# Kernel optimization log

Hardware: AMD Instinct MI355X
Metric: run time of the kernel (lower is better)

The kernel has to match this reference:

```python
import jax, jax.numpy as jnp
import numpy as np
import math

BATCH, SEQ, D_MODEL, D_EXPAND, D_STATE = 2, 1024, 512, 1024, 16


def setup_inputs() -> dict:
    key = jax.random.key(0)
    ks = jax.random.split(key, 12)
    x = jax.random.normal(ks[0], (BATCH, SEQ, D_MODEL), jnp.float32)

    def xavier(k, shape):
        fan_in, fan_out = shape[1], shape[0]
        lim = math.sqrt(6.0 / (fan_in + fan_out))
        return jax.random.uniform(k, shape, jnp.float32, -lim, lim)

    in_w = xavier(ks[1], (2 * D_EXPAND, D_MODEL))
    in_b = 0.1 * jax.random.normal(ks[2], (2 * D_EXPAND,), jnp.float32)
    out_w = xavier(ks[3], (D_MODEL, D_EXPAND))
    out_b = 0.1 * jax.random.normal(ks[4], (D_MODEL,), jnp.float32)
    ssm_w = xavier(ks[5], (4 * D_STATE + 1, D_EXPAND))
    ssm_b = 0.1 * jax.random.normal(ks[6], (4 * D_STATE + 1,), jnp.float32)
    # _init_weights: delta row gets tiny weights and a bias so softplus(bias)=0.1
    delta_bias = math.log(math.exp(0.1) - 1.0)
    ssm_w = ssm_w.at[4 * D_STATE:, :].set(1e-6)
    ssm_b = ssm_b.at[4 * D_STATE:].set(delta_bias)
    A_log_re = jnp.log(jax.random.uniform(ks[7], (D_EXPAND, D_STATE), jnp.float32) * 0.5 + 0.5)
    A_log_im = jnp.zeros((D_EXPAND, D_STATE), jnp.float32)
    D = jax.random.normal(ks[8], (D_EXPAND,), jnp.float32)
    return {"x": x, "in_w": in_w, "in_b": in_b, "ssm_w": ssm_w, "ssm_b": ssm_b,
            "out_w": out_w, "out_b": out_b, "A_log_re": A_log_re, "A_log_im": A_log_im, "D": D}


def _forward(x, in_w, in_b, ssm_w, ssm_b, out_w, out_b, A_log_re, A_log_im, D):
    bsz = x.shape[0]
    E, S = A_log_re.shape
    proj = x @ in_w.T + in_b                      # (B,L,2E)
    gate, x_ssm = jnp.split(proj, 2, axis=-1)
    gate = jax.nn.silu(gate)
    p = x_ssm @ ssm_w.T + ssm_b                   # (B,L,4S+1)
    B_re, B_im, C_re, C_im, delta = jnp.split(p, [S, 2 * S, 3 * S, 4 * S], axis=-1)
    C = C_re + 1j * C_im                          # (B,L,S)
    delta = jax.nn.softplus(delta)                # (B,L,1)
    A = A_log_re + 1j * A_log_im                  # (E,S)
    delta_c = delta[..., None].astype(jnp.complex64)  # (B,L,1,1)
    dA = delta_c * A                              # (B,L,E,S)
    A_bar = jnp.exp(dA)
    eps = jnp.finfo(jnp.float32).eps
    B_bar_large = delta_c * (A_bar - 1.0) / (dA + eps)
    B_bar_small = delta_c * (1.0 + dA / 2.0)
    B_bar = jnp.where(jnp.abs(dA) < 1e-3, B_bar_small, B_bar_large)  # (B,L,E,S)

    # sequential diagonal recurrence over time: h = A_bar_t * h + B_bar_t * x_t
    h0 = jnp.zeros((bsz, E, S), jnp.complex64)
    xs = (jnp.swapaxes(A_bar, 0, 1), jnp.swapaxes(B_bar, 0, 1),
          jnp.swapaxes(x_ssm, 0, 1), jnp.swapaxes(C, 0, 1))

    def step(h, inp):
        A_t, Bb_t, xs_t, C_t = inp
        h = A_t * h + Bb_t * xs_t[:, :, None]                       # (B,E,S)
        y_t = jnp.sum(h * jnp.conj(C_t)[:, None, :], axis=-1).real  # (B,E)
        return h, y_t

    _, ys = jax.lax.scan(step, h0, xs)            # ys: (L,B,E)
    y = jnp.swapaxes(ys, 0, 1)                    # (B,L,E)
    y = y + x_ssm * D
    return (y * gate) @ out_w.T + out_b           # (B,L,d_model)


def reference(x, in_w, in_b, ssm_w, ssm_b, out_w, out_b, A_log_re, A_log_im, D):
    return _forward(x, in_w, in_b, ssm_w, ssm_b, out_w, out_b, A_log_re, A_log_im, D)
```

## Files before the change

### kernel.cpp

```cpp
#include <hip/hip_runtime.h>
#include <hip/hip_bf16.h>
#include <stdint.h>


constexpr int B_ = 2, L_ = 1024, DM = 512, E_ = 1024, S_ = 16;
constexpr int BL = B_ * L_;
constexpr int BE = B_ * E_;
constexpr int PC = 32;
constexpr int NC = 64, CT = 16;
constexpr int CHAINS = S_ * BE;
constexpr int NPAD = 2176;

typedef float f32x4 __attribute__((ext_vector_type(4)));
typedef __bf16 bf16x8 __attribute__((ext_vector_type(8)));
typedef unsigned int u32x4 __attribute__((ext_vector_type(4)));
typedef unsigned short u16;
typedef u16 u16x4 __attribute__((ext_vector_type(4)));

#define DEVI __device__ __forceinline__

DEVI void gload_lds16(const void* g, void* l) {
  __builtin_amdgcn_global_load_lds(
      (__attribute__((address_space(1))) unsigned int*)(uintptr_t)g,
      (__attribute__((address_space(3))) unsigned int*)l, 16, 0, 0);
}
DEVI float rcp_fast(float x) { return __builtin_amdgcn_rcpf(x); }
DEVI float exp2_fast(float x) { return __builtin_amdgcn_exp2f(x); }
DEVI float softplus_f(float z) { return (z > 15.f) ? z : log1pf(__expf(z)); }
DEVI u16 bfc(float f) {
  __hip_bfloat16 h = __float2bfloat16(f);
  return __builtin_bit_cast(u16, h);
}
DEVI float bf2f(u16 u) {
  unsigned int x = ((unsigned int)u) << 16;
  return __builtin_bit_cast(float, x);
}
constexpr float L2E = 1.44269504f;

DEVI void cvt4(const float* s, u16* d) {
  f32x4 v = *(const f32x4*)s;
  u16x4 o = {bfc(v[0]), bfc(v[1]), bfc(v[2]), bfc(v[3])};
  *(u16x4*)d = o;
}
constexpr int R0 = 262144;
constexpr int R1 = R0 + 262144;
constexpr int R2 = R1 + 131072;
constexpr int R3 = R2 + 14208;
constexpr int R4 = R3 + 512;
constexpr int R5 = R4 + 28;
constexpr int W2B = 32;
constexpr int CVT_BLK = (R5 + 255) / 256;
__global__ __launch_bounds__(256) void prep(
    const float* __restrict__ x, const float* __restrict__ in_w,
    const float* __restrict__ out_w, const float* __restrict__ in_b,
    const float* __restrict__ ssm_w, float* __restrict__ part,
    u16* __restrict__ x_bf, u16* __restrict__ wc_bf,
    u16* __restrict__ outw_bf, float* __restrict__ bias_c) {
  const int tid = threadIdx.x;
  const int blk = blockIdx.x;
  if (blk < W2B) {
    const int ks = blk >> 1, q = blk & 1;
    __shared__ float wsl[17][64];
    for (int i = tid; i < 17 * 64; i += 256) {
      const int j = i >> 6, e = i & 63;
      const int srcrow = (j < 16) ? (32 + j) : 64;
      wsl[j][e] = ssm_w[(size_t)srcrow * 1024 + ks * 64 + e];
    }
    __syncthreads();
    const int col = q * 256 + tid;
    float acc[17] = {};
    const float* iw = in_w + (size_t)(1024 + ks * 64) * 512 + col;
#pragma unroll 4
    for (int e = 0; e < 64; ++e) {
      const float v = iw[(size_t)e * 512];
#pragma unroll
      for (int j = 0; j < 17; ++j) acc[j] = fmaf(wsl[j][e], v, acc[j]);
    }
#pragma unroll
    for (int j = 0; j < 17; ++j)
      part[((size_t)ks * 17 + j) * 512 + col] = acc[j];
    return;
  }
  int i4 = (blk - W2B) * 256 + tid;
  if (i4 < R0) { cvt4(x + (size_t)i4 * 4, x_bf + (size_t)i4 * 4); return; }
  if (i4 < R1) { size_t m = (size_t)(i4 - R0) * 4; cvt4(in_w + m, wc_bf + m); return; }
  if (i4 < R2) { size_t m = (size_t)(i4 - R1) * 4; cvt4(out_w + m, outw_bf + m); return; }
  if (i4 < R3) {
    size_t m = (size_t)(i4 - R2) * 4;
    u16x4 z = {0, 0, 0, 0};
    *(u16x4*)(wc_bf + (size_t)2065 * 512 + m) = z;
    return;
  }
  if (i4 < R4) {
    size_t m = (size_t)(i4 - R3) * 4;
    *(f32x4*)(bias_c + m) = *(const f32x4*)(in_b + m);
    return;
  }
  if (i4 < R5) {
    int idx = (i4 - R4) * 4;
    for (int q = 0; q < 4; ++q) {
      int mm = 2065 + idx + q;
      if (mm < NPAD) bias_c[mm] = 0.f;
    }
  }
}

__global__ __launch_bounds__(256) void prep2(
    const float* __restrict__ part, const float* __restrict__ ssm_w,
    const float* __restrict__ in_b, const float* __restrict__ ssm_b,
    u16* __restrict__ wc_bf, float* __restrict__ bias_c) {
  const int tid = threadIdx.x, blk = blockIdx.x;
  if (blk < 34) {
    const int idx = blk * 256 + tid;
    const int j = idx >> 9, col = idx & 511;
    float s = 0.f;
#pragma unroll
    for (int ks = 0; ks < 16; ++ks)
      s += part[((size_t)ks * 17 + j) * 512 + col];
    wc_bf[(size_t)(2048 + j) * 512 + col] = bfc(s);
  } else {
    const int j = blk - 34;
    const int srcrow = (j < 16) ? (32 + j) : 64;
    __shared__ float red[256];
    float a = 0.f;
    for (int e = tid; e < 1024; e += 256)
      a = fmaf(ssm_w[(size_t)srcrow * 1024 + e], in_b[1024 + e], a);
    red[tid] = a;
    __syncthreads();
    for (int st = 128; st >= 1; st >>= 1) {
      if (tid < st) red[tid] += red[tid + st];
      __syncthreads();
    }
    if (tid == 0) bias_c[2048 + j] = red[0] + ssm_b[srcrow];
  }
}

template <int WR, int WC, int FM, int FN, int KDIM, int MODE>
__global__ __launch_bounds__(WR * WC * 64) void gemm_bt(
    const u16* __restrict__ A, const u16* __restrict__ Bm,
    const float* __restrict__ bias, float* __restrict__ o0,
    u16* __restrict__ o1, u16* __restrict__ o2) {
  constexpr int NW = WR * WC;
  constexpr int BM = WR * FM * 16, BN = WC * FN * 16;
  constexpr int nA = BM / 16, nB = BN / 16;
  __shared__ __align__(16) u16 smem[(BM + BN) * 32];
  u16* As = smem;
  u16* Bs = smem + BM * 32;

  const int tid = threadIdx.x, w = tid >> 6, lane = tid & 63;
  const int tm = blockIdx.x, tn = blockIdx.y;
  const int wr = w / WC, wc = w % WC;
  const int lr = lane & 15, kg = lane >> 4;
  const int srow = lane >> 2;
  const int kcol = (lane & 3) * 8;

  f32x4 acc[FM][FN] = {};

  for (int kk = 0; kk < KDIM; kk += 32) {
    for (int i = w; i < nA; i += NW)
      gload_lds16(A + (size_t)(tm * BM + i * 16 + srow) * KDIM + kk + kcol,
                  As + i * 512);
    for (int i = w; i < nB; i += NW)
      gload_lds16(Bm + (size_t)(tn * BN + i * 16 + srow) * KDIM + kk + kcol,
                  Bs + i * 512);
    __syncthreads();
    bf16x8 af[FM], bfr[FN];
#pragma unroll
    for (int mi = 0; mi < FM; ++mi)
      af[mi] = __builtin_bit_cast(
          bf16x8, *(const u32x4*)(As + (wr * FM * 16 + mi * 16 + lr) * 32 + kg * 8));
#pragma unroll
    for (int ni = 0; ni < FN; ++ni)
      bfr[ni] = __builtin_bit_cast(
          bf16x8, *(const u32x4*)(Bs + (wc * FN * 16 + ni * 16 + lr) * 32 + kg * 8));
#pragma unroll
    for (int mi = 0; mi < FM; ++mi)
#pragma unroll
      for (int ni = 0; ni < FN; ++ni)
        acc[mi][ni] = __builtin_amdgcn_mfma_f32_16x16x32_bf16(af[mi], bfr[ni],
                                                              acc[mi][ni], 0, 0, 0);
    __syncthreads();
  }

  const int r0 = tm * BM + wr * FM * 16 + (lane >> 4) * 4;
  const int c0 = tn * BN + wc * FN * 16 + (lane & 15);
#pragma unroll
  for (int mi = 0; mi < FM; ++mi) {
#pragma unroll
    for (int ni = 0; ni < FN; ++ni) {
#pragma unroll
      for (int j = 0; j < 4; ++j) {
        const int rg = r0 + mi * 16 + j;
        const int cg = c0 + ni * 16;
        float v = acc[mi][ni][j] + bias[cg];
        if constexpr (MODE == 0) {
          if (cg < E_) {
            o1[(size_t)rg * E_ + cg] = bfc(v * rcp_fast(1.0f + __expf(-v)));
          } else if (cg < 2 * E_) {
            o2[(size_t)rg * E_ + (cg - E_)] = bfc(v);
          } else if (cg < 2 * E_ + 17) {
            o0[(size_t)rg * PC + (cg - 2 * E_)] = v;
          }
        } else {
          o0[(size_t)rg * DM + cg] = v;
        }
      }
    }
  }
}

__global__ __launch_bounds__(256) void pass1(
    const float* __restrict__ p_ws, const u16* __restrict__ xs_bf,
    const float* __restrict__ A_re, float* __restrict__ Pws,
    float* __restrict__ Qws) {
  __shared__ float dl[CT];
  const int tid = threadIdx.x, bid = blockIdx.x;
  const int eblk = bid & 63, c = (bid >> 6) & 63, b = bid >> 12;
  const int row0 = b * L_ + c * CT;
  if (tid < CT) dl[tid] = softplus_f(p_ws[(size_t)(row0 + tid) * PC + 16]);
  __syncthreads();
  const int el = tid >> 4, s = tid & 15;
  const int e = eblk * 16 + el;
  const float Are = A_re[e * 16 + s];
  const float AreL = Are * L2E;
  const float invA = rcp_fast(fminf(Are, -1e-12f));
  float h = 0.f, dsum = 0.f;
#pragma unroll
  for (int t = 0; t < CT; ++t) {
    const float d = dl[t];
    dsum += d;
    const float a = exp2_fast(d * AreL);
    const float xv = bf2f(xs_bf[(size_t)(row0 + t) * E_ + e]);
    h = fmaf(a, h, (a - 1.f) * invA * xv);
  }
  const size_t o = (size_t)c * CHAINS + ((size_t)b * E_ + e) * 16 + s;
  Qws[o] = h;
  Pws[o] = exp2_fast(dsum * AreL);
}

__global__ __launch_bounds__(256) void pass1b(const float* __restrict__ Pws,
                                              float* __restrict__ Qws) {
  const int i = blockIdx.x * 256 + threadIdx.x;
  float h = 0.f;
#pragma unroll 4
  for (int c = 0; c < NC; ++c) {
    const size_t o = (size_t)c * CHAINS + i;
    const float p_ = Pws[o], q_ = Qws[o];
    Qws[o] = h;
    h = fmaf(p_, h, q_);
  }
}

__global__ __launch_bounds__(256) void pass2(
    const float* __restrict__ p_ws, const u16* __restrict__ xs_bf,
    const u16* __restrict__ gate_bf, const float* __restrict__ A_re,
    const float* __restrict__ Dvec, const float* __restrict__ h0ws,
    u16* __restrict__ ygbf) {
  __shared__ float dl[CT];
  __shared__ __align__(16) float cl[CT][16];
  const int tid = threadIdx.x, bid = blockIdx.x;
  const int es = bid & 3, c = (bid >> 2) & 63, b = bid >> 8;
  const int row0 = b * L_ + c * CT;
  const int e = es * 256 + tid;

  if (tid < CT) dl[tid] = softplus_f(p_ws[(size_t)(row0 + tid) * PC + 16]);
  {
    const int t = tid >> 4, s = tid & 15;
    cl[t][s] = p_ws[(size_t)(row0 + t) * PC + s];
  }
  __syncthreads();

  float AreL[16], invA[16], h[16];
  const size_t hb = (size_t)c * CHAINS + ((size_t)b * E_ + e) * 16;
#pragma unroll
  for (int s4 = 0; s4 < 4; ++s4) {
    const f32x4 h4 = *(const f32x4*)(h0ws + hb + s4 * 4);
#pragma unroll
    for (int k = 0; k < 4; ++k) h[s4 * 4 + k] = h4[k];
  }
#pragma unroll
  for (int s = 0; s < 16; ++s) {
    const float Are = A_re[e * 16 + s];
    AreL[s] = Are * L2E;
    invA[s] = rcp_fast(fminf(Are, -1e-12f));
  }
  const float Dv = Dvec[e];

  for (int t = 0; t < CT; ++t) {
    const float d = dl[t];
    const float xv = bf2f(xs_bf[(size_t)(row0 + t) * E_ + e]);
    float y = 0.f;
#pragma unroll
    for (int s4 = 0; s4 < 4; ++s4) {
      const f32x4 c4 = *(const f32x4*)&cl[t][s4 * 4];
#pragma unroll
      for (int k = 0; k < 4; ++k) {
        const int s = s4 * 4 + k;
        const float a = exp2_fast(d * AreL[s]);
        h[s] = fmaf(a, h[s], (a - 1.f) * invA[s] * xv);
        y = fmaf(h[s], c4[k], y);
      }
    }
    const float g = bf2f(gate_bf[(size_t)(row0 + t) * E_ + e]);
    ygbf[(size_t)(row0 + t) * E_ + e] = bfc(fmaf(xv, Dv, y) * g);
  }
}

extern "C" void kernel_launch(void* const* d_in, const int* in_sizes, int n_in,
                              void* d_out, int out_size, void* d_ws, size_t ws_size,
                              hipStream_t stream) {
  (void)in_sizes; (void)n_in; (void)out_size; (void)ws_size;
  const float* x     = (const float*)d_in[0];
  const float* in_w  = (const float*)d_in[1];
  const float* in_b  = (const float*)d_in[2];
  const float* ssm_w = (const float*)d_in[3];
  const float* ssm_b = (const float*)d_in[4];
  const float* out_w = (const float*)d_in[5];
  const float* out_b = (const float*)d_in[6];
  const float* A_re  = (const float*)d_in[7];
  const float* Dv    = (const float*)d_in[9];
  float* out = (float*)d_out;

  char* wsp = (char*)d_ws;
  auto alloc = [&](size_t bytes) {
    char* p = wsp; wsp += (bytes + 255) & ~(size_t)255; return p;
  };
  u16* x_bf     = (u16*)alloc((size_t)BL * DM * 2);
  u16* wc_bf    = (u16*)alloc((size_t)NPAD * DM * 2);
  u16* outw_bf  = (u16*)alloc((size_t)DM * E_ * 2);
  float* part   = (float*)alloc((size_t)16 * 17 * 512 * 4);
  float* bias_c = (float*)alloc((size_t)NPAD * 4);
  u16* gate_bf  = (u16*)alloc((size_t)BL * E_ * 2);
  u16* xs_bf    = (u16*)alloc((size_t)BL * E_ * 2);
  float* p_ws   = (float*)alloc((size_t)BL * PC * 4);
  float* Pws    = (float*)alloc((size_t)NC * CHAINS * 4);
  float* Qws    = (float*)alloc((size_t)NC * CHAINS * 4);
  u16* ygbf     = (u16*)alloc((size_t)BL * E_ * 2);

  prep<<<dim3(W2B + CVT_BLK), dim3(256), 0, stream>>>(
      x, in_w, out_w, in_b, ssm_w, part, x_bf, wc_bf, outw_bf, bias_c);
  prep2<<<dim3(51), dim3(256), 0, stream>>>(part, ssm_w, in_b, ssm_b,
                                            wc_bf, bias_c);
  gemm_bt<2, 2, 4, 2, 512, 0><<<dim3(BL / 128, NPAD / 64), dim3(256), 0, stream>>>(
      x_bf, wc_bf, bias_c, p_ws, gate_bf, xs_bf);
  pass1<<<dim3(B_ * NC * 64), dim3(256), 0, stream>>>(p_ws, xs_bf, A_re, Pws, Qws);
  pass1b<<<dim3(CHAINS / 256), dim3(256), 0, stream>>>(Pws, Qws);
  pass2<<<dim3(B_ * NC * 4), dim3(256), 0, stream>>>(
      p_ws, xs_bf, gate_bf, A_re, Dv, Qws, ygbf);
  gemm_bt<2, 2, 2, 2, 1024, 2><<<dim3(BL / 64, DM / 64), dim3(256), 0, stream>>>(
      ygbf, outw_bf, out_b, out, nullptr, nullptr);
}
```

Baseline: 89.80 us.

## Fuse all stages into one persistent kernel with software grid barriers

```diff
diff --git a/kernel.cpp b/kernel.cpp
--- a/kernel.cpp
+++ b/kernel.cpp
@@ -9,7 +9,8 @@
 constexpr int PC = 32;
 constexpr int NC = 64, CT = 16;
 constexpr int CHAINS = S_ * BE;
-constexpr int NPAD = 2176;
+constexpr int NPAD = 2112;
+constexpr int NB = 512;
 
 typedef float f32x4 __attribute__((ext_vector_type(4)));
 typedef __bf16 bf16x8 __attribute__((ext_vector_type(8)));
@@ -37,6 +38,19 @@
 }
 constexpr float L2E = 1.44269504f;
 
+DEVI void gridbar(unsigned* ctr, unsigned target) {
+  __syncthreads();
+  if (threadIdx.x == 0) {
+    __builtin_amdgcn_fence(__ATOMIC_RELEASE, "agent");
+    __hip_atomic_fetch_add(ctr, 1u, __ATOMIC_RELAXED, __HIP_MEMORY_SCOPE_AGENT);
+    while (__hip_atomic_load(ctr, __ATOMIC_RELAXED, __HIP_MEMORY_SCOPE_AGENT) <
+           target)
+      __builtin_amdgcn_s_sleep(2);
+  }
+  __syncthreads();
+  __builtin_amdgcn_fence(__ATOMIC_ACQUIRE, "agent");
+}
+
 DEVI void cvt4(const float* s, u16* d) {
   f32x4 v = *(const f32x4*)s;
   u16x4 o = {bfc(v[0]), bfc(v[1]), bfc(v[2]), bfc(v[3])};
@@ -45,110 +59,26 @@
 constexpr int R0 = 262144;
 constexpr int R1 = R0 + 262144;
 constexpr int R2 = R1 + 131072;
-constexpr int R3 = R2 + 14208;
+constexpr int R3 = R2 + 6016;
 constexpr int R4 = R3 + 512;
-constexpr int R5 = R4 + 28;
+constexpr int R5 = R4 + 12;
 constexpr int W2B = 32;
 constexpr int CVT_BLK = (R5 + 255) / 256;
-__global__ __launch_bounds__(256) void prep(
-    const float* __restrict__ x, const float* __restrict__ in_w,
-    const float* __restrict__ out_w, const float* __restrict__ in_b,
-    const float* __restrict__ ssm_w, float* __restrict__ part,
-    u16* __restrict__ x_bf, u16* __restrict__ wc_bf,
-    u16* __restrict__ outw_bf, float* __restrict__ bias_c) {
-  const int tid = threadIdx.x;
-  const int blk = blockIdx.x;
-  if (blk < W2B) {
-    const int ks = blk >> 1, q = blk & 1;
-    __shared__ float wsl[17][64];
-    for (int i = tid; i < 17 * 64; i += 256) {
-      const int j = i >> 6, e = i & 63;
-      const int srcrow = (j < 16) ? (32 + j) : 64;
-      wsl[j][e] = ssm_w[(size_t)srcrow * 1024 + ks * 64 + e];
-    }
-    __syncthreads();
-    const int col = q * 256 + tid;
-    float acc[17] = {};
-    const float* iw = in_w + (size_t)(1024 + ks * 64) * 512 + col;
-#pragma unroll 4
-    for (int e = 0; e < 64; ++e) {
-      const float v = iw[(size_t)e * 512];
-#pragma unroll
-      for (int j = 0; j < 17; ++j) acc[j] = fmaf(wsl[j][e], v, acc[j]);
-    }
-#pragma unroll
-    for (int j = 0; j < 17; ++j)
-      part[((size_t)ks * 17 + j) * 512 + col] = acc[j];
-    return;
-  }
-  int i4 = (blk - W2B) * 256 + tid;
-  if (i4 < R0) { cvt4(x + (size_t)i4 * 4, x_bf + (size_t)i4 * 4); return; }
-  if (i4 < R1) { size_t m = (size_t)(i4 - R0) * 4; cvt4(in_w + m, wc_bf + m); return; }
-  if (i4 < R2) { size_t m = (size_t)(i4 - R1) * 4; cvt4(out_w + m, outw_bf + m); return; }
-  if (i4 < R3) {
-    size_t m = (size_t)(i4 - R2) * 4;
-    u16x4 z = {0, 0, 0, 0};
-    *(u16x4*)(wc_bf + (size_t)2065 * 512 + m) = z;
-    return;
-  }
-  if (i4 < R4) {
-    size_t m = (size_t)(i4 - R3) * 4;
-    *(f32x4*)(bias_c + m) = *(const f32x4*)(in_b + m);
-    return;
-  }
-  if (i4 < R5) {
-    int idx = (i4 - R4) * 4;
-    for (int q = 0; q < 4; ++q) {
-      int mm = 2065 + idx + q;
-      if (mm < NPAD) bias_c[mm] = 0.f;
-    }
-  }
-}
-
-__global__ __launch_bounds__(256) void prep2(
-    const float* __restrict__ part, const float* __restrict__ ssm_w,
-    const float* __restrict__ in_b, const float* __restrict__ ssm_b,
-    u16* __restrict__ wc_bf, float* __restrict__ bias_c) {
-  const int tid = threadIdx.x, blk = blockIdx.x;
-  if (blk < 34) {
-    const int idx = blk * 256 + tid;
-    const int j = idx >> 9, col = idx & 511;
-    float s = 0.f;
-#pragma unroll
-    for (int ks = 0; ks < 16; ++ks)
-      s += part[((size_t)ks * 17 + j) * 512 + col];
-    wc_bf[(size_t)(2048 + j) * 512 + col] = bfc(s);
-  } else {
-    const int j = blk - 34;
-    const int srcrow = (j < 16) ? (32 + j) : 64;
-    __shared__ float red[256];
-    float a = 0.f;
-    for (int e = tid; e < 1024; e += 256)
-      a = fmaf(ssm_w[(size_t)srcrow * 1024 + e], in_b[1024 + e], a);
-    red[tid] = a;
-    __syncthreads();
-    for (int st = 128; st >= 1; st >>= 1) {
-      if (tid < st) red[tid] += red[tid + st];
-      __syncthreads();
-    }
-    if (tid == 0) bias_c[2048 + j] = red[0] + ssm_b[srcrow];
-  }
-}
-
-template <int WR, int WC, int FM, int FN, int KDIM, int MODE>
-__global__ __launch_bounds__(WR * WC * 64) void gemm_bt(
-    const u16* __restrict__ A, const u16* __restrict__ Bm,
-    const float* __restrict__ bias, float* __restrict__ o0,
-    u16* __restrict__ o1, u16* __restrict__ o2) {
+constexpr int P0_VB = W2B + CVT_BLK;
+
+template <int WR, int WC, int FM, int FN, int KDIM, int MODE, int TN>
+DEVI void gemm_body(int vb, int tid, char* smem_raw,
+                    const u16* __restrict__ A, const u16* __restrict__ Bm,
+                    const float* __restrict__ bias, float* __restrict__ o0,
+                    u16* __restrict__ o1, u16* __restrict__ o2) {
   constexpr int NW = WR * WC;
   constexpr int BM = WR * FM * 16, BN = WC * FN * 16;
   constexpr int nA = BM / 16, nB = BN / 16;
-  __shared__ __align__(16) u16 smem[(BM + BN) * 32];
-  u16* As = smem;
-  u16* Bs = smem + BM * 32;
-
-  const int tid = threadIdx.x, w = tid >> 6, lane = tid & 63;
-  const int tm = blockIdx.x, tn = blockIdx.y;
+  u16* As = (u16*)smem_raw;
+  u16* Bs = As + BM * 32;
+
+  const int w = tid >> 6, lane = tid & 63;
+  const int tm = vb / TN, tn = vb % TN;
   const int wr = w / WC, wc = w % WC;
   const int lr = lane & 15, kg = lane >> 4;
   const int srow = lane >> 2;
@@ -209,101 +139,191 @@
   }
 }
 
-__global__ __launch_bounds__(256) void pass1(
-    const float* __restrict__ p_ws, const u16* __restrict__ xs_bf,
-    const float* __restrict__ A_re, float* __restrict__ Pws,
-    float* __restrict__ Qws) {
-  __shared__ float dl[CT];
-  const int tid = threadIdx.x, bid = blockIdx.x;
-  const int eblk = bid & 63, c = (bid >> 6) & 63, b = bid >> 12;
-  const int row0 = b * L_ + c * CT;
-  if (tid < CT) dl[tid] = softplus_f(p_ws[(size_t)(row0 + tid) * PC + 16]);
-  __syncthreads();
-  const int el = tid >> 4, s = tid & 15;
-  const int e = eblk * 16 + el;
-  const float Are = A_re[e * 16 + s];
-  const float AreL = Are * L2E;
-  const float invA = rcp_fast(fminf(Are, -1e-12f));
-  float h = 0.f, dsum = 0.f;
-#pragma unroll
-  for (int t = 0; t < CT; ++t) {
-    const float d = dl[t];
-    dsum += d;
-    const float a = exp2_fast(d * AreL);
-    const float xv = bf2f(xs_bf[(size_t)(row0 + t) * E_ + e]);
-    h = fmaf(a, h, (a - 1.f) * invA * xv);
-  }
-  const size_t o = (size_t)c * CHAINS + ((size_t)b * E_ + e) * 16 + s;
-  Qws[o] = h;
-  Pws[o] = exp2_fast(dsum * AreL);
-}
-
-__global__ __launch_bounds__(256) void pass1b(const float* __restrict__ Pws,
-                                              float* __restrict__ Qws) {
-  const int i = blockIdx.x * 256 + threadIdx.x;
-  float h = 0.f;
+__global__ __launch_bounds__(256, 2) void mega(
+    const float* __restrict__ x, const float* __restrict__ in_w,
+    const float* __restrict__ in_b, const float* __restrict__ ssm_w,
+    const float* __restrict__ ssm_b, const float* __restrict__ out_w,
+    const float* __restrict__ out_b, const float* __restrict__ A_re,
+    const float* __restrict__ Dvec, float* __restrict__ out,
+    u16* __restrict__ x_bf, u16* __restrict__ wc_bf, u16* __restrict__ outw_bf,
+    float* __restrict__ part, float* __restrict__ bias_c,
+    u16* __restrict__ gate_bf, u16* __restrict__ xs_bf,
+    float* __restrict__ p_ws, float* __restrict__ Pws, float* __restrict__ Qws,
+    u16* __restrict__ ygbf, unsigned* __restrict__ bar) {
+  __shared__ __align__(16) char smem_raw[12288];
+  const int r = blockIdx.x, tid = threadIdx.x;
+
+  for (int vb = r; vb < P0_VB; vb += NB) {
+    if (vb < W2B) {
+      const int ks = vb >> 1, q = vb & 1;
+      float* wsl = (float*)smem_raw;
+      for (int i = tid; i < 17 * 64; i += 256) {
+        const int j = i >> 6, e = i & 63;
+        const int srcrow = (j < 16) ? (32 + j) : 64;
+        wsl[j * 64 + e] = ssm_w[(size_t)srcrow * 1024 + ks * 64 + e];
+      }
+      __syncthreads();
+      const int col = q * 256 + tid;
+      float acc[17] = {};
+      const float* iw = in_w + (size_t)(1024 + ks * 64) * 512 + col;
 #pragma unroll 4
-  for (int c = 0; c < NC; ++c) {
-    const size_t o = (size_t)c * CHAINS + i;
-    const float p_ = Pws[o], q_ = Qws[o];
+      for (int e = 0; e < 64; ++e) {
+        const float v = iw[(size_t)e * 512];
+#pragma unroll
+        for (int j = 0; j < 17; ++j) acc[j] = fmaf(wsl[j * 64 + e], v, acc[j]);
+      }
+#pragma unroll
+      for (int j = 0; j < 17; ++j)
+        part[((size_t)ks * 17 + j) * 512 + col] = acc[j];
+      __syncthreads();
+      continue;
+    }
+    int i4 = (vb - W2B) * 256 + tid;
+    if (i4 < R0) { cvt4(x + (size_t)i4 * 4, x_bf + (size_t)i4 * 4); continue; }
+    if (i4 < R1) { size_t m = (size_t)(i4 - R0) * 4; cvt4(in_w + m, wc_bf + m); continue; }
+    if (i4 < R2) { size_t m = (size_t)(i4 - R1) * 4; cvt4(out_w + m, outw_bf + m); continue; }
+    if (i4 < R3) {
+      size_t m = (size_t)(i4 - R2) * 4;
+      u16x4 z = {0, 0, 0, 0};
+      *(u16x4*)(wc_bf + (size_t)2065 * 512 + m) = z;
+      continue;
+    }
+    if (i4 < R4) {
+      size_t m = (size_t)(i4 - R3) * 4;
+      *(f32x4*)(bias_c + m) = *(const f32x4*)(in_b + m);
+      continue;
+    }
+    if (i4 < R5) {
+      int idx = (i4 - R4) * 4;
+      for (int q = 0; q < 4; ++q) {
+        int mm = 2065 + idx + q;
+        if (mm < NPAD) bias_c[mm] = 0.f;
+      }
+    }
+  }
+  gridbar(bar + 0, NB);
+
+  if (r < 34) {
+    const int idx = r * 256 + tid;
+    const int j = idx >> 9, col = idx & 511;
+    float s = 0.f;
+#pragma unroll
+    for (int ks = 0; ks < 16; ++ks) s += part[((size_t)ks * 17 + j) * 512 + col];
+    wc_bf[(size_t)(2048 + j) * 512 + col] = bfc(s);
+  } else if (r < 51) {
+    const int j = r - 34;
+    const int srcrow = (j < 16) ? (32 + j) : 64;
+    float* red = (float*)smem_raw;
+    float a = 0.f;
+    for (int e = tid; e < 1024; e += 256)
+      a = fmaf(ssm_w[(size_t)srcrow * 1024 + e], in_b[1024 + e], a);
+    red[tid] = a;
+    __syncthreads();
+    for (int st = 128; st >= 1; st >>= 1) {
+      if (tid < st) red[tid] += red[tid + st];
+      __syncthreads();
+    }
+    if (tid == 0) bias_c[2048 + j] = red[0] + ssm_b[srcrow];
+  }
+  gridbar(bar + 1, NB);
+
+  for (int vb = r; vb < 16 * 33; vb += NB)
+    gemm_body<2, 2, 4, 2, 512, 0, 33>(vb, tid, smem_raw, x_bf, wc_bf, bias_c,
+                                      p_ws, gate_bf, xs_bf);
+  gridbar(bar + 2, NB);
+
+  for (int vb = r; vb < B_ * NC * 64; vb += NB) {
+    float* dl = (float*)smem_raw;
+    const int eblk = vb & 63, c = (vb >> 6) & 63, b = vb >> 12;
+    const int row0 = b * L_ + c * CT;
+    if (tid < CT) dl[tid] = softplus_f(p_ws[(size_t)(row0 + tid) * PC + 16]);
+    __syncthreads();
+    const int el = tid >> 4, s = tid & 15;
+    const int e = eblk * 16 + el;
+    const float Are = A_re[e * 16 + s];
+    const float AreL = Are * L2E;
+    const float invA = rcp_fast(fminf(Are, -1e-12f));
+    float h = 0.f, dsum = 0.f;
+#pragma unroll
+    for (int t = 0; t < CT; ++t) {
+      const float d = dl[t];
+      dsum += d;
+      const float a = exp2_fast(d * AreL);
+      const float xv = bf2f(xs_bf[(size_t)(row0 + t) * E_ + e]);
+      h = fmaf(a, h, (a - 1.f) * invA * xv);
+    }
+    const size_t o = (size_t)c * CHAINS + ((size_t)b * E_ + e) * 16 + s;
     Qws[o] = h;
-    h = fmaf(p_, h, q_);
-  }
-}
-
-__global__ __launch_bounds__(256) void pass2(
-    const float* __restrict__ p_ws, const u16* __restrict__ xs_bf,
-    const u16* __restrict__ gate_bf, const float* __restrict__ A_re,
-    const float* __restrict__ Dvec, const float* __restrict__ h0ws,
-    u16* __restrict__ ygbf) {
-  __shared__ float dl[CT];
-  __shared__ __align__(16) float cl[CT][16];
-  const int tid = threadIdx.x, bid = blockIdx.x;
-  const int es = bid & 3, c = (bid >> 2) & 63, b = bid >> 8;
-  const int row0 = b * L_ + c * CT;
-  const int e = es * 256 + tid;
-
-  if (tid < CT) dl[tid] = softplus_f(p_ws[(size_t)(row0 + tid) * PC + 16]);
+    Pws[o] = exp2_fast(dsum * AreL);
+    __syncthreads();
+  }
+  gridbar(bar + 3, NB);
+
+  if (tid < 64) {
+    const int i = r * 64 + tid;
+    float h = 0.f;
+#pragma unroll 4
+    for (int c = 0; c < NC; ++c) {
+      const size_t o = (size_t)c * CHAINS + i;
+      const float p_ = Pws[o], q_ = Qws[o];
+      Qws[o] = h;
+      h = fmaf(p_, h, q_);
+    }
+  }
+  gridbar(bar + 4, NB);
+
   {
-    const int t = tid >> 4, s = tid & 15;
-    cl[t][s] = p_ws[(size_t)(row0 + t) * PC + s];
-  }
-  __syncthreads();
-
-  float AreL[16], invA[16], h[16];
-  const size_t hb = (size_t)c * CHAINS + ((size_t)b * E_ + e) * 16;
-#pragma unroll
-  for (int s4 = 0; s4 < 4; ++s4) {
-    const f32x4 h4 = *(const f32x4*)(h0ws + hb + s4 * 4);
-#pragma unroll
-    for (int k = 0; k < 4; ++k) h[s4 * 4 + k] = h4[k];
-  }
-#pragma unroll
-  for (int s = 0; s < 16; ++s) {
-    const float Are = A_re[e * 16 + s];
-    AreL[s] = Are * L2E;
-    invA[s] = rcp_fast(fminf(Are, -1e-12f));
-  }
-  const float Dv = Dvec[e];
-
-  for (int t = 0; t < CT; ++t) {
-    const float d = dl[t];
-    const float xv = bf2f(xs_bf[(size_t)(row0 + t) * E_ + e]);
-    float y = 0.f;
+    float* dl = (float*)smem_raw;
+    float* cl = (float*)smem_raw + 16;
+    const int es = r & 3, c = (r >> 2) & 63, b = r >> 8;
+    const int row0 = b * L_ + c * CT;
+    const int e = es * 256 + tid;
+    if (tid < CT) dl[tid] = softplus_f(p_ws[(size_t)(row0 + tid) * PC + 16]);
+    {
+      const int t = tid >> 4, s = tid & 15;
+      cl[t * 16 + s] = p_ws[(size_t)(row0 + t) * PC + s];
+    }
+    __syncthreads();
+
+    float AreL[16], invA[16], h[16];
+    const size_t hb = (size_t)c * CHAINS + ((size_t)b * E_ + e) * 16;
 #pragma unroll
     for (int s4 = 0; s4 < 4; ++s4) {
-      const f32x4 c4 = *(const f32x4*)&cl[t][s4 * 4];
-#pragma unroll
-      for (int k = 0; k < 4; ++k) {
-        const int s = s4 * 4 + k;
-        const float a = exp2_fast(d * AreL[s]);
-        h[s] = fmaf(a, h[s], (a - 1.f) * invA[s] * xv);
-        y = fmaf(h[s], c4[k], y);
-      }
-    }
-    const float g = bf2f(gate_bf[(size_t)(row0 + t) * E_ + e]);
-    ygbf[(size_t)(row0 + t) * E_ + e] = bfc(fmaf(xv, Dv, y) * g);
-  }
+      const f32x4 h4 = *(const f32x4*)(Qws + hb + s4 * 4);
+#pragma unroll
+      for (int k = 0; k < 4; ++k) h[s4 * 4 + k] = h4[k];
+    }
+#pragma unroll
+    for (int s = 0; s < 16; ++s) {
+      const float Are = A_re[e * 16 + s];
+      AreL[s] = Are * L2E;
+      invA[s] = rcp_fast(fminf(Are, -1e-12f));
+    }
+    const float Dv = Dvec[e];
+
+    for (int t = 0; t < CT; ++t) {
+      const float d = dl[t];
+      const float xv = bf2f(xs_bf[(size_t)(row0 + t) * E_ + e]);
+      float y = 0.f;
+#pragma unroll
+      for (int s4 = 0; s4 < 4; ++s4) {
+        const f32x4 c4 = *(const f32x4*)(cl + t * 16 + s4 * 4);
+#pragma unroll
+        for (int k = 0; k < 4; ++k) {
+          const int s = s4 * 4 + k;
+          const float a = exp2_fast(d * AreL[s]);
+          h[s] = fmaf(a, h[s], (a - 1.f) * invA[s] * xv);
+          y = fmaf(h[s], c4[k], y);
+        }
+      }
+      const float g = bf2f(gate_bf[(size_t)(row0 + t) * E_ + e]);
+      ygbf[(size_t)(row0 + t) * E_ + e] = bfc(fmaf(xv, Dv, y) * g);
+    }
+  }
+  gridbar(bar + 5, NB);
+
+  gemm_body<2, 2, 2, 1, 1024, 2, 16>(r, tid, smem_raw, ygbf, outw_bf, out_b,
+                                     out, nullptr, nullptr);
 }
 
 extern "C" void kernel_launch(void* const* d_in, const int* in_sizes, int n_in,
@@ -336,17 +356,11 @@
   float* Pws    = (float*)alloc((size_t)NC * CHAINS * 4);
   float* Qws    = (float*)alloc((size_t)NC * CHAINS * 4);
   u16* ygbf     = (u16*)alloc((size_t)BL * E_ * 2);
-
-  prep<<<dim3(W2B + CVT_BLK), dim3(256), 0, stream>>>(
-      x, in_w, out_w, in_b, ssm_w, part, x_bf, wc_bf, outw_bf, bias_c);
-  prep2<<<dim3(51), dim3(256), 0, stream>>>(part, ssm_w, in_b, ssm_b,
-                                            wc_bf, bias_c);
-  gemm_bt<2, 2, 4, 2, 512, 0><<<dim3(BL / 128, NPAD / 64), dim3(256), 0, stream>>>(
-      x_bf, wc_bf, bias_c, p_ws, gate_bf, xs_bf);
-  pass1<<<dim3(B_ * NC * 64), dim3(256), 0, stream>>>(p_ws, xs_bf, A_re, Pws, Qws);
-  pass1b<<<dim3(CHAINS / 256), dim3(256), 0, stream>>>(Pws, Qws);
-  pass2<<<dim3(B_ * NC * 4), dim3(256), 0, stream>>>(
-      p_ws, xs_bf, gate_bf, A_re, Dv, Qws, ygbf);
-  gemm_bt<2, 2, 2, 2, 1024, 2><<<dim3(BL / 64, DM / 64), dim3(256), 0, stream>>>(
-      ygbf, outw_bf, out_b, out, nullptr, nullptr);
-}
+  unsigned* bar = (unsigned*)alloc(64);
+
+  hipMemsetAsync(bar, 0, 64, stream);
+  mega<<<dim3(NB), dim3(256), 0, stream>>>(
+      x, in_w, in_b, ssm_w, ssm_b, out_w, out_b, A_re, Dv, out,
+      x_bf, wc_bf, outw_bf, part, bias_c, gate_bf, xs_bf, p_ws, Pws, Qws,
+      ygbf, bar);
+}
```

New measurement: 355.2 us. +295.6%, slower.

## Trim padded projection width, move bias reduction into prep, stage xs in LDS

Applied to the files above, without the earlier changes.

```diff
diff --git a/kernel.cpp b/kernel.cpp
--- a/kernel.cpp
+++ b/kernel.cpp
@@ -9,10 +9,11 @@
 constexpr int PC = 32;
 constexpr int NC = 64, CT = 16;
 constexpr int CHAINS = S_ * BE;
-constexpr int NPAD = 2176;
+constexpr int NPAD = 2112;
 
 typedef float f32x4 __attribute__((ext_vector_type(4)));
 typedef __bf16 bf16x8 __attribute__((ext_vector_type(8)));
+typedef unsigned int u32;
 typedef unsigned int u32x4 __attribute__((ext_vector_type(4)));
 typedef unsigned short u16;
 typedef u16 u16x4 __attribute__((ext_vector_type(4)));
@@ -32,7 +33,7 @@
   return __builtin_bit_cast(u16, h);
 }
 DEVI float bf2f(u16 u) {
-  unsigned int x = ((unsigned int)u) << 16;
+  u32 x = ((u32)u) << 16;
   return __builtin_bit_cast(float, x);
 }
 constexpr float L2E = 1.44269504f;
@@ -45,16 +46,17 @@
 constexpr int R0 = 262144;
 constexpr int R1 = R0 + 262144;
 constexpr int R2 = R1 + 131072;
-constexpr int R3 = R2 + 14208;
+constexpr int R3 = R2 + 6016;
 constexpr int R4 = R3 + 512;
-constexpr int R5 = R4 + 28;
+constexpr int R5 = R4 + 12;
 constexpr int W2B = 32;
+constexpr int BIASB = 17;
 constexpr int CVT_BLK = (R5 + 255) / 256;
 __global__ __launch_bounds__(256) void prep(
     const float* __restrict__ x, const float* __restrict__ in_w,
     const float* __restrict__ out_w, const float* __restrict__ in_b,
-    const float* __restrict__ ssm_w, float* __restrict__ part,
-    u16* __restrict__ x_bf, u16* __restrict__ wc_bf,
+    const float* __restrict__ ssm_w, const float* __restrict__ ssm_b,
+    float* __restrict__ part, u16* __restrict__ x_bf, u16* __restrict__ wc_bf,
     u16* __restrict__ outw_bf, float* __restrict__ bias_c) {
   const int tid = threadIdx.x;
   const int blk = blockIdx.x;
@@ -81,45 +83,8 @@
       part[((size_t)ks * 17 + j) * 512 + col] = acc[j];
     return;
   }
-  int i4 = (blk - W2B) * 256 + tid;
-  if (i4 < R0) { cvt4(x + (size_t)i4 * 4, x_bf + (size_t)i4 * 4); return; }
-  if (i4 < R1) { size_t m = (size_t)(i4 - R0) * 4; cvt4(in_w + m, wc_bf + m); return; }
-  if (i4 < R2) { size_t m = (size_t)(i4 - R1) * 4; cvt4(out_w + m, outw_bf + m); return; }
-  if (i4 < R3) {
-    size_t m = (size_t)(i4 - R2) * 4;
-    u16x4 z = {0, 0, 0, 0};
-    *(u16x4*)(wc_bf + (size_t)2065 * 512 + m) = z;
-    return;
-  }
-  if (i4 < R4) {
-    size_t m = (size_t)(i4 - R3) * 4;
-    *(f32x4*)(bias_c + m) = *(const f32x4*)(in_b + m);
-    return;
-  }
-  if (i4 < R5) {
-    int idx = (i4 - R4) * 4;
-    for (int q = 0; q < 4; ++q) {
-      int mm = 2065 + idx + q;
-      if (mm < NPAD) bias_c[mm] = 0.f;
-    }
-  }
-}
-
-__global__ __launch_bounds__(256) void prep2(
-    const float* __restrict__ part, const float* __restrict__ ssm_w,
-    const float* __restrict__ in_b, const float* __restrict__ ssm_b,
-    u16* __restrict__ wc_bf, float* __restrict__ bias_c) {
-  const int tid = threadIdx.x, blk = blockIdx.x;
-  if (blk < 34) {
-    const int idx = blk * 256 + tid;
-    const int j = idx >> 9, col = idx & 511;
-    float s = 0.f;
-#pragma unroll
-    for (int ks = 0; ks < 16; ++ks)
-      s += part[((size_t)ks * 17 + j) * 512 + col];
-    wc_bf[(size_t)(2048 + j) * 512 + col] = bfc(s);
-  } else {
-    const int j = blk - 34;
+  if (blk < W2B + BIASB) {
+    const int j = blk - W2B;
     const int srcrow = (j < 16) ? (32 + j) : 64;
     __shared__ float red[256];
     float a = 0.f;
@@ -132,7 +97,41 @@
       __syncthreads();
     }
     if (tid == 0) bias_c[2048 + j] = red[0] + ssm_b[srcrow];
-  }
+    return;
+  }
+  int i4 = (blk - W2B - BIASB) * 256 + tid;
+  if (i4 < R0) { cvt4(x + (size_t)i4 * 4, x_bf + (size_t)i4 * 4); return; }
+  if (i4 < R1) { size_t m = (size_t)(i4 - R0) * 4; cvt4(in_w + m, wc_bf + m); return; }
+  if (i4 < R2) { size_t m = (size_t)(i4 - R1) * 4; cvt4(out_w + m, outw_bf + m); return; }
+  if (i4 < R3) {
+    size_t m = (size_t)(i4 - R2) * 4;
+    u16x4 z = {0, 0, 0, 0};
+    *(u16x4*)(wc_bf + (size_t)2065 * 512 + m) = z;
+    return;
+  }
+  if (i4 < R4) {
+    size_t m = (size_t)(i4 - R3) * 4;
+    *(f32x4*)(bias_c + m) = *(const f32x4*)(in_b + m);
+    return;
+  }
+  if (i4 < R5) {
+    int idx = (i4 - R4) * 4;
+    for (int q = 0; q < 4; ++q) {
+      int mm = 2065 + idx + q;
+      if (mm < NPAD) bias_c[mm] = 0.f;
+    }
+  }
+}
+
+__global__ __launch_bounds__(256) void prep2(const float* __restrict__ part,
+                                             u16* __restrict__ wc_bf) {
+  const int idx = blockIdx.x * 256 + threadIdx.x;
+  const int j = idx >> 9, col = idx & 511;
+  float s = 0.f;
+#pragma unroll
+  for (int ks = 0; ks < 16; ++ks)
+    s += part[((size_t)ks * 17 + j) * 512 + col];
+  wc_bf[(size_t)(2048 + j) * 512 + col] = bfc(s);
 }
 
 template <int WR, int WC, int FM, int FN, int KDIM, int MODE>
@@ -214,13 +213,19 @@
     const float* __restrict__ A_re, float* __restrict__ Pws,
     float* __restrict__ Qws) {
   __shared__ float dl[CT];
+  __shared__ u16 xsl[CT][16];
   const int tid = threadIdx.x, bid = blockIdx.x;
   const int eblk = bid & 63, c = (bid >> 6) & 63, b = bid >> 12;
   const int row0 = b * L_ + c * CT;
+  const int e0 = eblk * 16;
   if (tid < CT) dl[tid] = softplus_f(p_ws[(size_t)(row0 + tid) * PC + 16]);
+  {
+    const int t = tid >> 4, q = tid & 15;
+    xsl[t][q] = xs_bf[(size_t)(row0 + t) * E_ + e0 + q];
+  }
   __syncthreads();
   const int el = tid >> 4, s = tid & 15;
-  const int e = eblk * 16 + el;
+  const int e = e0 + el;
   const float Are = A_re[e * 16 + s];
   const float AreL = Are * L2E;
   const float invA = rcp_fast(fminf(Are, -1e-12f));
@@ -230,8 +235,7 @@
     const float d = dl[t];
     dsum += d;
     const float a = exp2_fast(d * AreL);
-    const float xv = bf2f(xs_bf[(size_t)(row0 + t) * E_ + e]);
-    h = fmaf(a, h, (a - 1.f) * invA * xv);
+    h = fmaf(a, h, (a - 1.f) * invA * bf2f(xsl[t][el]));
   }
   const size_t o = (size_t)c * CHAINS + ((size_t)b * E_ + e) * 16 + s;
   Qws[o] = h;
@@ -337,10 +341,9 @@
   float* Qws    = (float*)alloc((size_t)NC * CHAINS * 4);
   u16* ygbf     = (u16*)alloc((size_t)BL * E_ * 2);
 
-  prep<<<dim3(W2B + CVT_BLK), dim3(256), 0, stream>>>(
-      x, in_w, out_w, in_b, ssm_w, part, x_bf, wc_bf, outw_bf, bias_c);
-  prep2<<<dim3(51), dim3(256), 0, stream>>>(part, ssm_w, in_b, ssm_b,
-                                            wc_bf, bias_c);
+  prep<<<dim3(W2B + BIASB + CVT_BLK), dim3(256), 0, stream>>>(
+      x, in_w, out_w, in_b, ssm_w, ssm_b, part, x_bf, wc_bf, outw_bf, bias_c);
+  prep2<<<dim3(34), dim3(256), 0, stream>>>(part, wc_bf);
   gemm_bt<2, 2, 4, 2, 512, 0><<<dim3(BL / 128, NPAD / 64), dim3(256), 0, stream>>>(
       x_bf, wc_bf, bias_c, p_ws, gate_bf, xs_bf);
   pass1<<<dim3(B_ * NC * 64), dim3(256), 0, stream>>>(p_ws, xs_bf, A_re, Pws, Qws);
```

Result: no change. 88.54 us (median of 2 runs) (-1.4%).
